# Kernel tuning notes

Measured on AMD Instinct MI355X. Metric: run time of the kernel, lower is better.

## Reference

```python
import jax, jax.numpy as jnp
import numpy as np

NUM_EXPERTS = 64
TOP_K = 2
CAP_FACTOR = 1.0


def setup_inputs() -> dict:
    key = jax.random.key(0)
    k1, k2 = jax.random.split(key)
    x = jax.random.normal(k1, (8192, 4096), dtype=jnp.float32)
    wg = jax.random.normal(k2, (NUM_EXPERTS, 4096), dtype=jnp.float32) * 0.02
    return {"x": x, "wg": wg}


def reference(x, wg):
    # x: [S, M] tokens, wg: [E, M] gate weight (Linear, no bias)
    S, M = x.shape
    E, K = NUM_EXPERTS, TOP_K
    capacity = K * int(CAP_FACTOR * ((S + E - 1) // E))  # static

    logits = jnp.einsum('sm,em->se', x, wg)            # [S, E]
    gates = jax.nn.softmax(logits, axis=1)             # [S, E]
    _, topk_idx = jax.lax.top_k(logits, K)             # [S, K]

    masks = jax.nn.one_hot(topk_idx, E, dtype=x.dtype)  # [S, K, E]
    gates_s = jnp.einsum('se,ske->sk', gates, masks)    # [S, K]

    # load-balancing loss (fp32 path of load_balance)
    me = jnp.sum(gates, axis=0)                         # [E]
    ce = jnp.sum(masks[:, 0], axis=0)                   # [E]
    l_loss = jnp.sum(me * ce) * (E / (S * S))

    # capacity locations: cumsum-sub-one per k, offset by counts of earlier k's
    locs = jnp.cumsum(masks, axis=0) - 1.0              # [S, K, E]
    counts = jnp.sum(masks, axis=0)                     # [K, E]
    acc = jnp.concatenate([jnp.zeros((1, E), x.dtype),
                           jnp.cumsum(counts, axis=0)[:-1]], axis=0)  # [K, E]
    locs = locs + acc[None, :, :]
    loc_s = jnp.einsum('ske,ske->sk', locs, masks).astype(jnp.int32)  # [S, K]

    # postnorm gate normalization (top_k > 1)
    eps = jnp.finfo(gates_s.dtype).eps
    gates_n = gates_s / jnp.clip(jnp.sum(gates_s, axis=1, keepdims=True), eps)

    idx = topk_idx.astype(jnp.int32)                    # [S, K]
    valid = (loc_s >= 0) & (loc_s < capacity)           # [S, K]
    pos = jnp.where(valid, idx * capacity + loc_s, 0)   # [S, K] flat slot ids

    # encode: scatter tokens (unweighted, is_postnorm=True) into [E*capacity, M]
    contrib = jnp.where(valid[..., None], x[:, None, :], 0.0)  # [S, K, M]
    dispatched = jnp.zeros((E * capacity, M), x.dtype)
    dispatched = dispatched.at[pos.reshape(-1)].add(contrib.reshape(-1, M))

    # expert_fn = identity (world_size=1, routing pipeline is the op under test)
    expert_output = dispatched                          # [E*capacity, M]

    # decode: gather back and combine with normalized gates
    gathered = expert_output[pos.reshape(-1)].reshape(S, K, M)
    out = jnp.einsum('sk,skm->sm', gates_n * valid.astype(x.dtype), gathered)
    return out, l_loss
```

## Files before the change

### kernel.cpp

```cpp
#include <hip/hip_runtime.h>
#include <math.h>
#include <stdint.h>

#define S_TOK 8192
#define M_DIM 4096
#define NEXP 64
#define CAPACITY 256
#define NCHUNK 128
#define KS 16
#define KSL 256
#define BT 256
#define BK 32
#define NC (KSL / BK)

__global__ __launch_bounds__(256) void k_wt(
    const float* __restrict__ wg, float* __restrict__ wgT)
{
    const int k = blockIdx.x * 4 + (threadIdx.x >> 6);
    const int e = threadIdx.x & 63;
    wgT[(size_t)k * NEXP + e] = wg[(size_t)e * M_DIM + k];
}

__global__ __launch_bounds__(256, 2) void k_logits(
    const float* __restrict__ x, const float* __restrict__ wgT,
    float* __restrict__ part)
{
    __shared__ float xs[2][BK * BT];
    __shared__ float ws[2][BK * NEXP];
    const int tid = threadIdx.x;
    const int tile = blockIdx.x >> 4;
    const int ks   = blockIdx.x & 15;
    const int t0 = tile * BT;
    const int kb = ks * KSL;

    const int wv = tid >> 6, lane = tid & 63;
    const int tx = tid & 7;
    const int ty = tid >> 3;

    auto stage = [&](int buf, int kc) {
        #pragma unroll
        for (int q = 0; q < 8; ++q) {
            const int r = wv * 8 + q;
            const int tok = r * 8 + (lane >> 3);
            const int bsrc = (lane & 7) ^ (r & 7);
            __builtin_amdgcn_global_load_lds(
                (const __attribute__((address_space(1))) void*)
                    (x + (size_t)(t0 + tok) * M_DIM + kc + 4 * bsrc),
                (__attribute__((address_space(3))) void*)(&xs[buf][r * 256]),
                16, 0, 0);
        }
        #pragma unroll
        for (int q = 0; q < 2; ++q) {
            const int rw = wv * 2 + q;
            __builtin_amdgcn_global_load_lds(
                (const __attribute__((address_space(1))) void*)
                    (wgT + (size_t)kc * NEXP + rw * 256 + lane * 4),
                (__attribute__((address_space(3))) void*)(&ws[buf][rw * 256]),
                16, 0, 0);
        }
    };

    float acc[8][8] = {};
    stage(0, kb);
    __syncthreads();

    for (int c = 0; c < NC; ++c) {
        const int buf = c & 1;
        if (c + 1 < NC) stage(buf ^ 1, kb + (c + 1) * BK);

        const float* xb = xs[buf];
        const float* wb = ws[buf];
        #pragma unroll
        for (int kq = 0; kq < BK / 4; ++kq) {
            float4 al[8];
            #pragma unroll
            for (int i = 0; i < 8; ++i) {
                const int tok = 8 * ty + i;
                al[i] = *(const float4*)&xb[tok * 32 + ((kq ^ (ty & 7)) << 2)];
            }
            float4 bl[4], bh[4];
            #pragma unroll
            for (int kk = 0; kk < 4; ++kk) {
                bl[kk] = *(const float4*)&wb[(4 * kq + kk) * NEXP + 8 * tx];
                bh[kk] = *(const float4*)&wb[(4 * kq + kk) * NEXP + 8 * tx + 4];
            }
            #pragma unroll
            for (int kk = 0; kk < 4; ++kk) {
                const float bj[8] = {bl[kk].x, bl[kk].y, bl[kk].z, bl[kk].w,
                                     bh[kk].x, bh[kk].y, bh[kk].z, bh[kk].w};
                #pragma unroll
                for (int i = 0; i < 8; ++i) {
                    const float ai = ((const float*)&al[i])[kk];
                    #pragma unroll
                    for (int j = 0; j < 8; ++j)
                        acc[i][j] = fmaf(ai, bj[j], acc[i][j]);
                }
            }
        }
        __syncthreads();
    }

    #pragma unroll
    for (int i = 0; i < 8; ++i) {
        float4 v0, v1;
        v0.x = acc[i][0]; v0.y = acc[i][1]; v0.z = acc[i][2]; v0.w = acc[i][3];
        v1.x = acc[i][4]; v1.y = acc[i][5]; v1.z = acc[i][6]; v1.w = acc[i][7];
        float* dst = part + ((size_t)ks * S_TOK + t0 + 8 * ty + i) * NEXP + 8 * tx;
        *(float4*)dst = v0;
        *(float4*)(dst + 4) = v1;
    }
}

__global__ __launch_bounds__(512) void k_gate(
    const float* __restrict__ part, float* __restrict__ me_g,
    int* __restrict__ idx0_g, int* __restrict__ idx1_g,
    float* __restrict__ gn0_g, float* __restrict__ gn1_g,
    int* __restrict__ rank0_g, int* __restrict__ rank1_g,
    int* __restrict__ cnt_g )
{
    __shared__ float me_sh[NEXP];
    __shared__ int e0_sh[64], e1_sh[64];
    const int tid = threadIdx.x;
    if (tid < NEXP) me_sh[tid] = 0.f;
    __syncthreads();

    const int wv = tid >> 6, lane = tid & 63;
    const int chunk = blockIdx.x;
    float me_acc = 0.f;
    for (int i = 0; i < 8; ++i) {
        const int tt = wv * 8 + i;
        const int t = chunk * 64 + tt;
        float lg = 0.f;
        #pragma unroll
        for (int s = 0; s < KS; ++s)
            lg += part[((size_t)s * S_TOK + t) * NEXP + lane];

        float v = lg; int id = lane;
        #pragma unroll
        for (int off = 32; off > 0; off >>= 1) {
            float v2 = __shfl_xor(v, off);
            int   i2 = __shfl_xor(id, off);
            if (v2 > v || (v2 == v && i2 < id)) { v = v2; id = i2; }
        }
        const float mx = v; const int i0 = id;

        const float p = expf(lg - mx);
        float sum = p;
        #pragma unroll
        for (int off = 32; off > 0; off >>= 1) sum += __shfl_xor(sum, off);
        me_acc += p / sum;

        float v1 = (lane == i0) ? -INFINITY : lg; int id1 = lane;
        #pragma unroll
        for (int off = 32; off > 0; off >>= 1) {
            float v2 = __shfl_xor(v1, off);
            int   i2 = __shfl_xor(id1, off);
            if (v2 > v1 || (v2 == v1 && i2 < id1)) { v1 = v2; id1 = i2; }
        }

        const float g0 = 1.0f / sum;
        const float g1 = expf(v1 - mx) / sum;
        const float den = fmaxf(g0 + g1, 1.1920929e-07f);
        if (lane == 0) {
            idx0_g[t] = i0;
            idx1_g[t] = id1;
            gn0_g[t] = g0 / den;
            gn1_g[t] = g1 / den;
            e0_sh[tt] = i0;
            e1_sh[tt] = id1;
        }
    }
    atomicAdd(&me_sh[lane], me_acc);
    __syncthreads();
    if (tid < NEXP) atomicAdd(&me_g[tid], me_sh[tid]);

    if (wv == 0) {
        const int s = chunk * 64 + lane;
        const int e0 = e0_sh[lane], e1 = e1_sh[lane];
        const unsigned long long lt = (1ull << lane) - 1ull;
        int r0 = 0, r1 = 0, c0 = 0, c1 = 0;
        #pragma unroll
        for (int e = 0; e < 64; ++e) {
            unsigned long long m0 = __ballot(e0 == e);
            unsigned long long m1 = __ballot(e1 == e);
            if (e0 == e) r0 = __popcll(m0 & lt);
            if (e1 == e) r1 = __popcll(m1 & lt);
            if (lane == e) { c0 = __popcll(m0); c1 = __popcll(m1); }
        }
        rank0_g[s] = r0;
        rank1_g[s] = r1;
        cnt_g[chunk * 64 + lane] = c0;
        cnt_g[NCHUNK * 64 + chunk * 64 + lane] = c1;
    }
}

__global__ __launch_bounds__(256) void k_scan(
    const int* __restrict__ cnt_g, int* __restrict__ base_g,
    int* __restrict__ tot0_g, const float* __restrict__ me_g,
    float* __restrict__ loss_out)
{
    const int wv = threadIdx.x >> 6, lane = threadIdx.x & 63;
    const int g = blockIdx.x * 4 + wv;
    const int k = g >> 6, e = g & 63;

    const int c0 = cnt_g[(k * NCHUNK + 2 * lane)     * 64 + e];
    const int c1 = cnt_g[(k * NCHUNK + 2 * lane + 1) * 64 + e];
    const int s = c0 + c1;
    int incl = s;
    #pragma unroll
    for (int d = 1; d < 64; d <<= 1) {
        int v = __shfl_up(incl, d);
        if (lane >= d) incl += v;
    }
    const int excl = incl - s;
    base_g[(k * NCHUNK + 2 * lane)     * 64 + e] = excl;
    base_g[(k * NCHUNK + 2 * lane + 1) * 64 + e] = excl + c0;
    const int total = __shfl(incl, 63);
    if (k == 0 && lane == 0) {
        tot0_g[e] = total;
        atomicAdd(loss_out, me_g[e] * (float)total * 9.5367431640625e-07f);
    }
}

__global__ __launch_bounds__(256) void k_out(
    const float* __restrict__ x,
    const int* __restrict__ idx0_g, const int* __restrict__ idx1_g,
    const float* __restrict__ gn0_g, const float* __restrict__ gn1_g,
    const int* __restrict__ rank0_g, const int* __restrict__ rank1_g,
    const int* __restrict__ base_g, const int* __restrict__ tot0_g,
    float* __restrict__ out)
{
    const int s = blockIdx.x;
    const int chunk = s >> 6;
    const int e0 = idx0_g[s], e1 = idx1_g[s];
    const int loc0 = base_g[chunk * 64 + e0] + rank0_g[s];
    const int loc1 = base_g[(NCHUNK + chunk) * 64 + e1] + rank1_g[s] + tot0_g[e1];
    float w = 0.f;
    if (loc0 < CAPACITY) w += gn0_g[s];
    if (loc1 < CAPACITY) w += gn1_g[s];

    const float4* xr = (const float4*)(x + (size_t)s * M_DIM);
    float4* o = (float4*)(out + (size_t)s * M_DIM);
    #pragma unroll
    for (int i = 0; i < 4; ++i) {
        float4 v = xr[threadIdx.x + 256 * i];
        v.x *= w; v.y *= w; v.z *= w; v.w *= w;
        o[threadIdx.x + 256 * i] = v;
    }
}

extern "C" void kernel_launch(void* const* d_in, const int* in_sizes, int n_in,
                              void* d_out, int out_size, void* d_ws, size_t ws_size,
                              hipStream_t stream)
{
    const float* x  = (const float*)d_in[0];
    const float* wg = (const float*)d_in[1];
    float* out = (float*)d_out;
    float* loss = out + (size_t)S_TOK * M_DIM;

    float* part = (float*)d_ws;
    float* me   = part + (size_t)KS * S_TOK * NEXP;
    int*  idx0  = (int*)(me + NEXP);
    int*  idx1  = idx0 + S_TOK;
    float* gn0  = (float*)(idx1 + S_TOK);
    float* gn1  = gn0 + S_TOK;
    int*  rank0 = (int*)(gn1 + S_TOK);
    int*  rank1 = rank0 + S_TOK;
    int*  cnt   = rank1 + S_TOK;
    int*  base  = cnt + 2 * NCHUNK * 64;
    int*  tot0  = base + 2 * NCHUNK * 64;
    float* wgT  = (float*)(tot0 + NEXP);

    hipMemsetAsync(me, 0, NEXP * sizeof(float), stream);
    hipMemsetAsync(loss, 0, sizeof(float), stream);

    k_wt<<<M_DIM / 4, 256, 0, stream>>>(wg, wgT);
    k_logits<<<32 * KS, 256, 0, stream>>>(x, wgT, part);
    k_gate<<<NCHUNK, 512, 0, stream>>>(part, me, idx0, idx1, gn0, gn1,
                                       rank0, rank1, cnt);
    k_scan<<<32, 256, 0, stream>>>(cnt, base, tot0, me, loss);
    k_out<<<S_TOK, 256, 0, stream>>>(x, idx0, idx1, gn0, gn1,
                                     rank0, rank1, base, tot0, out);
}
```

Measured before the change: 357.2 us.

## Restructure logits GEMM: halve token tile, read gate weights via wave-uniform scalar loads

The logits kernel tile shrinks from 256 to 128 tokens, which doubles the grid. Each thread now owns one token and 32 experts instead of an 8x8 register tile. The gate weights are no longer staged in LDS: a wave-uniform expert-group index lets the compiler fetch weight rows through scalar loads, so only x goes through LDS. This removes the weight staging and the LDS reads for B. In exchange, every x value is reused across only 32 experts per thread, and scalar-load latency may stall the FMAs.

```diff
diff --git a/kernel.cpp b/kernel.cpp
--- a/kernel.cpp
+++ b/kernel.cpp
@@ -9,7 +9,7 @@
 #define NCHUNK 128
 #define KS 16
 #define KSL 256
-#define BT 256
+#define BT 128
 #define BK 32
 #define NC (KSL / BK)
 
@@ -21,93 +21,71 @@
     wgT[(size_t)k * NEXP + e] = wg[(size_t)e * M_DIM + k];
 }
 
-__global__ __launch_bounds__(256, 2) void k_logits(
+__global__ __launch_bounds__(256) void k_logits(
     const float* __restrict__ x, const float* __restrict__ wgT,
     float* __restrict__ part)
 {
-    __shared__ float xs[2][BK * BT];
-    __shared__ float ws[2][BK * NEXP];
+    __shared__ float xs[2][BT * BK];
     const int tid = threadIdx.x;
     const int tile = blockIdx.x >> 4;
     const int ks   = blockIdx.x & 15;
     const int t0 = tile * BT;
     const int kb = ks * KSL;
 
-    const int wv = tid >> 6, lane = tid & 63;
-    const int tx = tid & 7;
-    const int ty = tid >> 3;
+    const int lane = tid & 63;
+    const int wv = __builtin_amdgcn_readfirstlane(tid >> 6);
+    const int tg = wv >> 1;
+    const int eg = wv & 1;
+    const int tok_l = tg * 64 + lane;
 
     auto stage = [&](int buf, int kc) {
         #pragma unroll
-        for (int q = 0; q < 8; ++q) {
-            const int r = wv * 8 + q;
-            const int tok = r * 8 + (lane >> 3);
-            const int bsrc = (lane & 7) ^ (r & 7);
+        for (int i = 0; i < 4; ++i) {
+            const int item = tid + 256 * i;
+            const int tok = item >> 3;
+            const int kqp = item & 7;
+            const int kqs = kqp ^ (tok & 7);
             __builtin_amdgcn_global_load_lds(
                 (const __attribute__((address_space(1))) void*)
-                    (x + (size_t)(t0 + tok) * M_DIM + kc + 4 * bsrc),
-                (__attribute__((address_space(3))) void*)(&xs[buf][r * 256]),
+                    (x + (size_t)(t0 + tok) * M_DIM + kc + 4 * kqs),
+                (__attribute__((address_space(3))) void*)(&xs[buf][item * 4]),
                 16, 0, 0);
         }
-        #pragma unroll
-        for (int q = 0; q < 2; ++q) {
-            const int rw = wv * 2 + q;
-            __builtin_amdgcn_global_load_lds(
-                (const __attribute__((address_space(1))) void*)
-                    (wgT + (size_t)kc * NEXP + rw * 256 + lane * 4),
-                (__attribute__((address_space(3))) void*)(&ws[buf][rw * 256]),
-                16, 0, 0);
-        }
     };
 
-    float acc[8][8] = {};
+    float acc[32] = {};
     stage(0, kb);
     __syncthreads();
 
     for (int c = 0; c < NC; ++c) {
         const int buf = c & 1;
-        if (c + 1 < NC) stage(buf ^ 1, kb + (c + 1) * BK);
-
-        const float* xb = xs[buf];
-        const float* wb = ws[buf];
-        #pragma unroll
-        for (int kq = 0; kq < BK / 4; ++kq) {
-            float4 al[8];
-            #pragma unroll
-            for (int i = 0; i < 8; ++i) {
-                const int tok = 8 * ty + i;
-                al[i] = *(const float4*)&xb[tok * 32 + ((kq ^ (ty & 7)) << 2)];
-            }
-            float4 bl[4], bh[4];
+        const int kc = kb + c * BK;
+        if (c + 1 < NC) stage(buf ^ 1, kc + BK);
+
+        #pragma unroll
+        for (int kq = 0; kq < 8; ++kq) {
+            const float4 a = *(const float4*)
+                &xs[buf][tok_l * BK + ((kq ^ (lane & 7)) << 2)];
+            const float av[4] = {a.x, a.y, a.z, a.w};
             #pragma unroll
             for (int kk = 0; kk < 4; ++kk) {
-                bl[kk] = *(const float4*)&wb[(4 * kq + kk) * NEXP + 8 * tx];
-                bh[kk] = *(const float4*)&wb[(4 * kq + kk) * NEXP + 8 * tx + 4];
+                const float* brow =
+                    wgT + (size_t)(kc + 4 * kq + kk) * NEXP + eg * 32;
+                #pragma unroll
+                for (int e = 0; e < 32; ++e)
+                    acc[e] = fmaf(brow[e], av[kk], acc[e]);
             }
-            #pragma unroll
-            for (int kk = 0; kk < 4; ++kk) {
-                const float bj[8] = {bl[kk].x, bl[kk].y, bl[kk].z, bl[kk].w,
-                                     bh[kk].x, bh[kk].y, bh[kk].z, bh[kk].w};
-                #pragma unroll
-                for (int i = 0; i < 8; ++i) {
-                    const float ai = ((const float*)&al[i])[kk];
-                    #pragma unroll
-                    for (int j = 0; j < 8; ++j)
-                        acc[i][j] = fmaf(ai, bj[j], acc[i][j]);
-                }
-            }
         }
         __syncthreads();
     }
 
+    float* dst = part + ((size_t)ks * S_TOK + t0 + tok_l) * NEXP + eg * 32;
     #pragma unroll
-    for (int i = 0; i < 8; ++i) {
-        float4 v0, v1;
-        v0.x = acc[i][0]; v0.y = acc[i][1]; v0.z = acc[i][2]; v0.w = acc[i][3];
-        v1.x = acc[i][4]; v1.y = acc[i][5]; v1.z = acc[i][6]; v1.w = acc[i][7];
-        float* dst = part + ((size_t)ks * S_TOK + t0 + 8 * ty + i) * NEXP + 8 * tx;
-        *(float4*)dst = v0;
-        *(float4*)(dst + 4) = v1;
+    for (int q = 0; q < 8; ++q) {
+        float4 v;
+        v.x = acc[4 * q];     v.y = acc[4 * q + 1];
+        v.z = acc[4 * q + 2]; v.w = acc[4 * q + 3];
+        *(float4*)(dst + 4 * q) = v;
     }
 }
 
@@ -275,7 +253,7 @@
     hipMemsetAsync(loss, 0, sizeof(float), stream);
 
     k_wt<<<M_DIM / 4, 256, 0, stream>>>(wg, wgT);
-    k_logits<<<32 * KS, 256, 0, stream>>>(x, wgT, part);
+    k_logits<<<(S_TOK / BT) * KS, 256, 0, stream>>>(x, wgT, part);
     k_gate<<<NCHUNK, 512, 0, stream>>>(part, me, idx0, idx1, gn0, gn1,
                                        rank0, rank1, cnt);
     k_scan<<<32, 256, 0, stream>>>(cnt, base, tot0, me, loss);
```

After: 324.2 us. 1.1x faster.
